# Kernel optimization log

Measured on AMD Instinct MI355X. Metric: run time of the kernel, lower is better.

Reference implementation:

```python
import jax, jax.numpy as jnp
import numpy as np

C1 = 0.01 ** 2
C2 = 0.03 ** 2
EPS = 1e-8


def _box3(t):
    # 3x3 mean filter, zero padding (SAME), NCHW, 1 channel.
    k = jnp.full((1, 1, 3, 3), 1.0 / 9.0, dtype=t.dtype)
    return jax.lax.conv_general_dilated(
        t, k, window_strides=(1, 1), padding=((1, 1), (1, 1)),
        dimension_numbers=("NCHW", "OIHW", "NCHW"))


def setup_inputs() -> dict:
    key = jax.random.key(0)
    k1, k2 = jax.random.split(key)
    shape = (32, 1, 1024, 1024)
    x = jax.random.uniform(k1, shape, dtype=jnp.float32)
    y = jax.random.uniform(k2, shape, dtype=jnp.float32)
    return {"x": x, "y": y}


def reference(x, y):
    mu_x = _box3(x)
    mu_y = _box3(y)
    sigma_x = _box3(x * x) - mu_x * mu_x
    sigma_y = _box3(y * y) - mu_y * mu_y
    sigma_xy = _box3(x * y) - mu_x * mu_y
    ssim_map = ((2.0 * mu_x * mu_y + C1) * (2.0 * sigma_xy + C2)
                / ((mu_x ** 2 + mu_y ** 2 + C1) * (sigma_x + sigma_y + C2) + EPS))
    return 1.0 - jnp.mean(ssim_map)
```

## Files before the change

### kernel.cpp

```cpp
#include <hip/hip_runtime.h>

#define IMG_H 1024
#define IMG_W 1024
#define RPB   16
#define TPB   256

struct HS { float x[4], y[4], xx[4], yy[4], xy[4]; };

__device__ __forceinline__ void zero_hs(HS& h)
{
#pragma unroll
    for (int j = 0; j < 4; ++j) { h.x[j]=0.f; h.y[j]=0.f; h.xx[j]=0.f; h.yy[j]=0.f; h.xy[j]=0.f; }
}

__device__ __forceinline__ void load_hs(const float* __restrict__ xr,
                                        const float* __restrict__ yr,
                                        int c, HS& h)
{
    float4 xv = *reinterpret_cast<const float4*>(xr + c);
    float4 yv = *reinterpret_cast<const float4*>(yr + c);
    float xs[6], ys[6];
    xs[0] = (c > 0) ? xr[c - 1] : 0.0f;
    ys[0] = (c > 0) ? yr[c - 1] : 0.0f;
    xs[1] = xv.x; xs[2] = xv.y; xs[3] = xv.z; xs[4] = xv.w;
    ys[1] = yv.x; ys[2] = yv.y; ys[3] = yv.z; ys[4] = yv.w;
    xs[5] = (c + 4 < IMG_W) ? xr[c + 4] : 0.0f;
    ys[5] = (c + 4 < IMG_W) ? yr[c + 4] : 0.0f;

    float pxx[6], pyy[6], pxy[6];
#pragma unroll
    for (int k = 0; k < 6; ++k) {
        pxx[k] = xs[k] * xs[k];
        pyy[k] = ys[k] * ys[k];
        pxy[k] = xs[k] * ys[k];
    }
#pragma unroll
    for (int j = 0; j < 4; ++j) {
        h.x[j]  = xs[j]  + xs[j + 1]  + xs[j + 2];
        h.y[j]  = ys[j]  + ys[j + 1]  + ys[j + 2];
        h.xx[j] = pxx[j] + pxx[j + 1] + pxx[j + 2];
        h.yy[j] = pyy[j] + pyy[j + 1] + pyy[j + 2];
        h.xy[j] = pxy[j] + pxy[j + 1] + pxy[j + 2];
    }
}

__device__ __forceinline__ void accum(const HS& A, const HS& B, const HS& C, float& acc)
{
    const float c1s  = 81.0f * 1e-4f;
    const float c2s  = 81.0f * 9e-4f;
    const float epss = 6561.0f * 1e-8f;
#pragma unroll
    for (int j = 0; j < 4; ++j) {
        const float sx  = A.x[j]  + B.x[j]  + C.x[j];
        const float sy  = A.y[j]  + B.y[j]  + C.y[j];
        const float sxx = A.xx[j] + B.xx[j] + C.xx[j];
        const float syy = A.yy[j] + B.yy[j] + C.yy[j];
        const float sxy = A.xy[j] + B.xy[j] + C.xy[j];

        const float t1 = sx * sy;
        const float t2 = fmaf(sx, sx, sy * sy);
        const float s2 = sxx + syy;
        const float An = fmaf(2.0f, t1, c1s);
        const float Bn = fmaf(-2.0f, t1, fmaf(18.0f, sxy, c2s));
        const float Xd = t2 + c1s;
        const float Yd = fmaf(9.0f, s2, c2s - t2);
        const float den = fmaf(Xd, Yd, epss);
        const float num = An * Bn;
        acc = fmaf(num, __builtin_amdgcn_rcpf(den), acc);
    }
}

__global__ __launch_bounds__(TPB)
void ssim_map_sum_kernel(const float* __restrict__ x,
                         const float* __restrict__ y,
                         float* __restrict__ ws_sum)
{
    const int rb = blockIdx.x;
    const int n  = blockIdx.y;
    const int r0 = rb * RPB;
    const int c  = (int)threadIdx.x * 4;

    const float* xi = x + (size_t)n * IMG_H * IMG_W;
    const float* yi = y + (size_t)n * IMG_H * IMG_W;

    HS hA, hB, hC;
    if (r0 > 0) load_hs(xi + (size_t)(r0 - 1) * IMG_W, yi + (size_t)(r0 - 1) * IMG_W, c, hA);
    else        zero_hs(hA);
    load_hs(xi + (size_t)r0 * IMG_W, yi + (size_t)r0 * IMG_W, c, hB);

    float acc = 0.0f;

    for (int i = 0; i < RPB; ++i) {
        const int r = r0 + i;
        if (r + 1 < IMG_H) {
            load_hs(xi + (size_t)(r + 1) * IMG_W, yi + (size_t)(r + 1) * IMG_W, c, hC);
        } else {
            zero_hs(hC);
        }

        accum(hA, hB, hC, acc);

#pragma unroll
        for (int j = 0; j < 4; ++j) {
            hA.x[j]=hB.x[j]; hA.y[j]=hB.y[j]; hA.xx[j]=hB.xx[j]; hA.yy[j]=hB.yy[j]; hA.xy[j]=hB.xy[j];
            hB.x[j]=hC.x[j]; hB.y[j]=hC.y[j]; hB.xx[j]=hC.xx[j]; hB.yy[j]=hC.yy[j]; hB.xy[j]=hC.xy[j];
        }
    }

#pragma unroll
    for (int off = 32; off > 0; off >>= 1)
        acc += __shfl_down(acc, off);

    __shared__ float red[TPB / 64];
    const int lane = (int)threadIdx.x & 63;
    const int wave = (int)threadIdx.x >> 6;
    if (lane == 0) red[wave] = acc;
    __syncthreads();
    if (threadIdx.x == 0) {
        float s = 0.0f;
#pragma unroll
        for (int w = 0; w < TPB / 64; ++w) s += red[w];
        atomicAdd(ws_sum, s);
    }
}

__global__ void ssim_finalize_kernel(const float* __restrict__ ws_sum,
                                     float* __restrict__ out,
                                     float inv_count)
{
    out[0] = 1.0f - ws_sum[0] * inv_count;
}

extern "C" void kernel_launch(void* const* d_in, const int* in_sizes, int n_in,
                              void* d_out, int out_size, void* d_ws, size_t ws_size,
                              hipStream_t stream)
{
    const float* x = (const float*)d_in[0];
    const float* y = (const float*)d_in[1];
    float* out  = (float*)d_out;
    float* wsum = (float*)d_ws;

    const long long total = (long long)in_sizes[0];
    const int N = (int)(total / ((long long)IMG_H * IMG_W));

    hipMemsetAsync(wsum, 0, sizeof(float), stream);

    dim3 grid(IMG_H / RPB, N);
    ssim_map_sum_kernel<<<grid, TPB, 0, stream>>>(x, y, wsum);

    ssim_finalize_kernel<<<1, 1, 0, stream>>>(wsum, out, 1.0f / (float)total);
}
```

Before: 297.5 us.

## Software-pipeline row loads one row ahead with branchless edge handling

New measurement: 461.4 us. 1.55x slower.

```diff
diff --git a/kernel.cpp b/kernel.cpp
--- a/kernel.cpp
+++ b/kernel.cpp
@@ -5,7 +5,8 @@
 #define RPB   16
 #define TPB   256
 
-struct HS { float x[4], y[4], xx[4], yy[4], xy[4]; };
+struct HS  { float x[4], y[4], xx[4], yy[4], xy[4]; };
+struct Raw { float x[6], y[6]; };
 
 __device__ __forceinline__ void zero_hs(HS& h)
 {
@@ -13,19 +14,25 @@
     for (int j = 0; j < 4; ++j) { h.x[j]=0.f; h.y[j]=0.f; h.xx[j]=0.f; h.yy[j]=0.f; h.xy[j]=0.f; }
 }
 
-__device__ __forceinline__ void load_hs(const float* __restrict__ xr,
-                                        const float* __restrict__ yr,
-                                        int c, HS& h)
+__device__ __forceinline__ void load_raw(const float* __restrict__ xr,
+                                         const float* __restrict__ yr,
+                                         int c, int cl, int cr, Raw& r)
 {
     float4 xv = *reinterpret_cast<const float4*>(xr + c);
     float4 yv = *reinterpret_cast<const float4*>(yr + c);
+    r.x[0] = xr[cl]; r.x[5] = xr[cr];
+    r.y[0] = yr[cl]; r.y[5] = yr[cr];
+    r.x[1] = xv.x; r.x[2] = xv.y; r.x[3] = xv.z; r.x[4] = xv.w;
+    r.y[1] = yv.x; r.y[2] = yv.y; r.y[3] = yv.z; r.y[4] = yv.w;
+}
+
+__device__ __forceinline__ void hsum(const Raw& r, float lm, float rm, HS& h)
+{
     float xs[6], ys[6];
-    xs[0] = (c > 0) ? xr[c - 1] : 0.0f;
-    ys[0] = (c > 0) ? yr[c - 1] : 0.0f;
-    xs[1] = xv.x; xs[2] = xv.y; xs[3] = xv.z; xs[4] = xv.w;
-    ys[1] = yv.x; ys[2] = yv.y; ys[3] = yv.z; ys[4] = yv.w;
-    xs[5] = (c + 4 < IMG_W) ? xr[c + 4] : 0.0f;
-    ys[5] = (c + 4 < IMG_W) ? yr[c + 4] : 0.0f;
+    xs[0] = r.x[0] * lm; ys[0] = r.y[0] * lm;
+    xs[5] = r.x[5] * rm; ys[5] = r.y[5] * rm;
+#pragma unroll
+    for (int k = 1; k < 5; ++k) { xs[k] = r.x[k]; ys[k] = r.y[k]; }
 
     float pxx[6], pyy[6], pxy[6];
 #pragma unroll
@@ -70,7 +77,7 @@
     }
 }
 
-__global__ __launch_bounds__(TPB)
+__global__ __launch_bounds__(TPB, 4)
 void ssim_map_sum_kernel(const float* __restrict__ x,
                          const float* __restrict__ y,
                          float* __restrict__ ws_sum)
@@ -80,32 +87,61 @@
     const int r0 = rb * RPB;
     const int c  = (int)threadIdx.x * 4;
 
+    const int   cl = (c > 0) ? c - 1 : 0;
+    const int   cr = (c + 4 < IMG_W) ? c + 4 : IMG_W - 1;
+    const float lm = (c > 0) ? 1.0f : 0.0f;
+    const float rm = (c + 4 < IMG_W) ? 1.0f : 0.0f;
+
     const float* xi = x + (size_t)n * IMG_H * IMG_W;
     const float* yi = y + (size_t)n * IMG_H * IMG_W;
 
     HS hA, hB, hC;
-    if (r0 > 0) load_hs(xi + (size_t)(r0 - 1) * IMG_W, yi + (size_t)(r0 - 1) * IMG_W, c, hA);
-    else        zero_hs(hA);
-    load_hs(xi + (size_t)r0 * IMG_W, yi + (size_t)r0 * IMG_W, c, hB);
+    Raw raw0, raw1;
+
+    if (r0 > 0) {
+        Raw rp;
+        load_raw(xi + (size_t)(r0 - 1) * IMG_W, yi + (size_t)(r0 - 1) * IMG_W, c, cl, cr, rp);
+        hsum(rp, lm, rm, hA);
+    } else {
+        zero_hs(hA);
+    }
+    {
+        Raw rq;
+        load_raw(xi + (size_t)r0 * IMG_W, yi + (size_t)r0 * IMG_W, c, cl, cr, rq);
+        hsum(rq, lm, rm, hB);
+    }
+    load_raw(xi + (size_t)(r0 + 1) * IMG_W, yi + (size_t)(r0 + 1) * IMG_W, c, cl, cr, raw0);
 
     float acc = 0.0f;
 
-    for (int i = 0; i < RPB; ++i) {
-        const int r = r0 + i;
-        if (r + 1 < IMG_H) {
-            load_hs(xi + (size_t)(r + 1) * IMG_W, yi + (size_t)(r + 1) * IMG_W, c, hC);
-        } else {
-            zero_hs(hC);
-        }
+#define STEP(P, Q, R, RIN, ROUT, k)                                               \
+    load_raw(xi + (size_t)(r0 + (k) + 2) * IMG_W,                                 \
+             yi + (size_t)(r0 + (k) + 2) * IMG_W, c, cl, cr, ROUT);               \
+    hsum(RIN, lm, rm, R);                                                         \
+    accum(P, Q, R, acc);
 
-        accum(hA, hB, hC, acc);
+    for (int ii = 0; ii < 12; ii += 6) {
+        STEP(hA, hB, hC, raw0, raw1, ii + 0)
+        STEP(hB, hC, hA, raw1, raw0, ii + 1)
+        STEP(hC, hA, hB, raw0, raw1, ii + 2)
+        STEP(hA, hB, hC, raw1, raw0, ii + 3)
+        STEP(hB, hC, hA, raw0, raw1, ii + 4)
+        STEP(hC, hA, hB, raw1, raw0, ii + 5)
+    }
+    STEP(hA, hB, hC, raw0, raw1, 12)
+    STEP(hB, hC, hA, raw1, raw0, 13)
+#undef STEP
 
-#pragma unroll
-        for (int j = 0; j < 4; ++j) {
-            hA.x[j]=hB.x[j]; hA.y[j]=hB.y[j]; hA.xx[j]=hB.xx[j]; hA.yy[j]=hB.yy[j]; hA.xy[j]=hB.xy[j];
-            hB.x[j]=hC.x[j]; hB.y[j]=hC.y[j]; hB.xx[j]=hC.xx[j]; hB.yy[j]=hC.yy[j]; hB.xy[j]=hC.xy[j];
-        }
+    {
+        const int rr = (r0 + 16 < IMG_H) ? r0 + 16 : IMG_H - 1;
+        load_raw(xi + (size_t)rr * IMG_W, yi + (size_t)rr * IMG_W, c, cl, cr, raw1);
+        hsum(raw0, lm, rm, hB);
+        accum(hC, hA, hB, acc);
     }
+
+    if (r0 + 16 < IMG_H) hsum(raw1, lm, rm, hC);
+    else                 zero_hs(hC);
+    accum(hA, hB, hC, acc);
 
 #pragma unroll
     for (int off = 32; off > 0; off >>= 1)
```

## Stage 2D tiles with halos in LDS and compute SSIM from shared memory

Applied to the files above, without the earlier changes.

New measurement: 419.0 us. 1.41x slower.

```diff
diff --git a/kernel.cpp b/kernel.cpp
--- a/kernel.cpp
+++ b/kernel.cpp
@@ -1,31 +1,27 @@
 #include <hip/hip_runtime.h>
 
-#define IMG_H 1024
-#define IMG_W 1024
-#define RPB   16
-#define TPB   256
+#define IMG_H  1024
+#define IMG_W  1024
+#define TILE_C 128
+#define RPB    16
+#define TPB    128
+#define SROWS  (RPB + 2)
+#define SCOL4  ((TILE_C + 8) / 4)
+#define SCOLS  (TILE_C + 8)
 
 struct HS { float x[4], y[4], xx[4], yy[4], xy[4]; };
 
-__device__ __forceinline__ void zero_hs(HS& h)
+__device__ __forceinline__ void hsum_lds(const float* __restrict__ rx,
+                                         const float* __restrict__ ry,
+                                         int j0, HS& h)
 {
-#pragma unroll
-    for (int j = 0; j < 4; ++j) { h.x[j]=0.f; h.y[j]=0.f; h.xx[j]=0.f; h.yy[j]=0.f; h.xy[j]=0.f; }
-}
-
-__device__ __forceinline__ void load_hs(const float* __restrict__ xr,
-                                        const float* __restrict__ yr,
-                                        int c, HS& h)
-{
-    float4 xv = *reinterpret_cast<const float4*>(xr + c);
-    float4 yv = *reinterpret_cast<const float4*>(yr + c);
     float xs[6], ys[6];
-    xs[0] = (c > 0) ? xr[c - 1] : 0.0f;
-    ys[0] = (c > 0) ? yr[c - 1] : 0.0f;
+    const float4 xv = *reinterpret_cast<const float4*>(rx + j0 + 4);
+    const float4 yv = *reinterpret_cast<const float4*>(ry + j0 + 4);
+    xs[0] = rx[j0 + 3]; ys[0] = ry[j0 + 3];
     xs[1] = xv.x; xs[2] = xv.y; xs[3] = xv.z; xs[4] = xv.w;
     ys[1] = yv.x; ys[2] = yv.y; ys[3] = yv.z; ys[4] = yv.w;
-    xs[5] = (c + 4 < IMG_W) ? xr[c + 4] : 0.0f;
-    ys[5] = (c + 4 < IMG_W) ? yr[c + 4] : 0.0f;
+    xs[5] = rx[j0 + 8]; ys[5] = ry[j0 + 8];
 
     float pxx[6], pyy[6], pxy[6];
 #pragma unroll
@@ -75,48 +71,62 @@
                          const float* __restrict__ y,
                          float* __restrict__ ws_sum)
 {
-    const int rb = blockIdx.x;
-    const int n  = blockIdx.y;
-    const int r0 = rb * RPB;
-    const int c  = (int)threadIdx.x * 4;
+    __shared__ float sx[SROWS][SCOLS];
+    __shared__ float sy[SROWS][SCOLS];
+
+    const int c0 = blockIdx.x * TILE_C;
+    const int r0 = blockIdx.y * RPB;
+    const int n  = blockIdx.z;
+    const int tid = (int)threadIdx.x;
 
     const float* xi = x + (size_t)n * IMG_H * IMG_W;
     const float* yi = y + (size_t)n * IMG_H * IMG_W;
 
-    HS hA, hB, hC;
-    if (r0 > 0) load_hs(xi + (size_t)(r0 - 1) * IMG_W, yi + (size_t)(r0 - 1) * IMG_W, c, hA);
-    else        zero_hs(hA);
-    load_hs(xi + (size_t)r0 * IMG_W, yi + (size_t)r0 * IMG_W, c, hB);
+    for (int idx = tid; idx < SROWS * SCOL4; idx += TPB) {
+        const int row = idx / SCOL4;
+        const int c4  = idx - row * SCOL4;
+        const int grow = r0 - 1 + row;
+        const int gcol = c0 - 4 + c4 * 4;
+        const int crow = min(max(grow, 0), IMG_H - 1);
+        const int ccol = min(max(gcol, 0), IMG_W - 4);
+        const float m = (grow >= 0 && grow < IMG_H && gcol >= 0 && gcol + 3 < IMG_W)
+                        ? 1.0f : 0.0f;
+        const float4 xv = *reinterpret_cast<const float4*>(xi + (size_t)crow * IMG_W + ccol);
+        const float4 yv = *reinterpret_cast<const float4*>(yi + (size_t)crow * IMG_W + ccol);
+        float* dx = &sx[row][c4 * 4];
+        float* dy = &sy[row][c4 * 4];
+        dx[0] = xv.x * m; dx[1] = xv.y * m; dx[2] = xv.z * m; dx[3] = xv.w * m;
+        dy[0] = yv.x * m; dy[1] = yv.y * m; dy[2] = yv.z * m; dy[3] = yv.w * m;
+    }
+    __syncthreads();
+
+    const int j0 = (tid & 31) * 4;
+    const int g  = (tid >> 5) * 4;
 
     float acc = 0.0f;
-
-    for (int i = 0; i < RPB; ++i) {
-        const int r = r0 + i;
-        if (r + 1 < IMG_H) {
-            load_hs(xi + (size_t)(r + 1) * IMG_W, yi + (size_t)(r + 1) * IMG_W, c, hC);
-        } else {
-            zero_hs(hC);
-        }
-
-        accum(hA, hB, hC, acc);
-
-#pragma unroll
-        for (int j = 0; j < 4; ++j) {
-            hA.x[j]=hB.x[j]; hA.y[j]=hB.y[j]; hA.xx[j]=hB.xx[j]; hA.yy[j]=hB.yy[j]; hA.xy[j]=hB.xy[j];
-            hB.x[j]=hC.x[j]; hB.y[j]=hC.y[j]; hB.xx[j]=hC.xx[j]; hB.yy[j]=hC.yy[j]; hB.xy[j]=hC.xy[j];
-        }
-    }
+    HS hA, hB, hC;
+    hsum_lds(sx[g + 0], sy[g + 0], j0, hA);
+    hsum_lds(sx[g + 1], sy[g + 1], j0, hB);
+    hsum_lds(sx[g + 2], sy[g + 2], j0, hC);
+    accum(hA, hB, hC, acc);
+    hsum_lds(sx[g + 3], sy[g + 3], j0, hA);
+    accum(hB, hC, hA, acc);
+    hsum_lds(sx[g + 4], sy[g + 4], j0, hB);
+    accum(hC, hA, hB, acc);
+    hsum_lds(sx[g + 5], sy[g + 5], j0, hC);
+    accum(hA, hB, hC, acc);
 
 #pragma unroll
     for (int off = 32; off > 0; off >>= 1)
         acc += __shfl_down(acc, off);
 
     __shared__ float red[TPB / 64];
-    const int lane = (int)threadIdx.x & 63;
-    const int wave = (int)threadIdx.x >> 6;
+    const int lane = tid & 63;
+    const int wave = tid >> 6;
+    __syncthreads();
     if (lane == 0) red[wave] = acc;
     __syncthreads();
-    if (threadIdx.x == 0) {
+    if (tid == 0) {
         float s = 0.0f;
 #pragma unroll
         for (int w = 0; w < TPB / 64; ++w) s += red[w];
@@ -145,7 +155,7 @@
 
     hipMemsetAsync(wsum, 0, sizeof(float), stream);
 
-    dim3 grid(IMG_H / RPB, N);
+    dim3 grid(IMG_W / TILE_C, IMG_H / RPB, N);
     ssim_map_sum_kernel<<<grid, TPB, 0, stream>>>(x, y, wsum);
 
     ssim_finalize_kernel<<<1, 1, 0, stream>>>(wsum, out, 1.0f / (float)total);
```
